# Kernel tuning notes

Hardware: AMD Instinct MI355X
Metric: run time of the kernel (lower is better)

## Reference

```python
import jax, jax.numpy as jnp
import numpy as np

NUM_HEADS = 12
NUM_GROUPS = 4
METRIC_SCALE = 1.0
CLS_MIX = 1.0
MEAN_MIX = 0.5
ROUTER_SCALE = 1.0
DIFF_SCALE = 1.0
B, N, D, HF = 16, 577, 768, 3072


def _ln(x, g, b, eps=1e-5):
    mu = jnp.mean(x, axis=-1, keepdims=True)
    var = jnp.mean(jnp.square(x - mu), axis=-1, keepdims=True)
    return (x - mu) * jax.lax.rsqrt(var + eps) * g + b


def setup_inputs() -> dict:
    key = jax.random.key(0)
    ks = iter(jax.random.split(key, 16))
    w = lambda shape, std: jax.random.normal(next(ks), shape, jnp.float32) * std
    return {
        "x": w((B, N, D), 1.0),
        "ln1_g": jnp.ones((D,)), "ln1_b": jnp.zeros((D,)),
        "ad_ln_g": jnp.ones((D,)), "ad_ln_b": jnp.zeros((D,)),
        "ad_w": w((D, D), 0.02),
        "w_qkv": w((D, 3 * D), 0.02),
        "w_proj": w((D, D), 0.02), "b_proj": jnp.zeros((D,)),
        "ln2_g": jnp.ones((D,)), "ln2_b": jnp.zeros((D,)),
        "fc1_w": w((D, HF), 0.02), "fc1_b": jnp.zeros((HF,)),
        "fc2_w": w((HF, D), 0.02), "fc2_b": jnp.zeros((D,)),
        "r_ln_g": jnp.ones((HF,)), "r_ln_b": jnp.zeros((HF,)),
        "r_proj_w": w((2 * HF, NUM_GROUPS), 0.02), "r_proj_b": jnp.zeros((NUM_GROUPS,)),
        "r_gate_w": w((2 * HF, 1), 0.02), "r_gate_b": jnp.full((1,), -2.0),
        "r_scale": jnp.full((NUM_GROUPS,), 0.1),
        "d_ln_g": jnp.ones((HF,)), "d_ln_b": jnp.zeros((HF,)),
        "d_out_w": w((HF, HF), 0.005),
        "d_gate_w": w((HF, 1), 0.02), "d_gate_b": jnp.full((1,), -1.5),
    }


def reference(x, ln1_g, ln1_b, ad_ln_g, ad_ln_b, ad_w, w_qkv, w_proj, b_proj,
              ln2_g, ln2_b, fc1_w, fc1_b, fc2_w, fc2_b,
              r_ln_g, r_ln_b, r_proj_w, r_proj_b, r_gate_w, r_gate_b, r_scale,
              d_ln_g, d_ln_b, d_out_w, d_gate_w, d_gate_b):
    b, n, d = x.shape
    hd = d // NUM_HEADS
    # ---- GeoAttention (pre-norm) ----
    h = _ln(x, ln1_g, ln1_b)
    # metric adapter: residual LN+Linear (SharedAttentionMetricAdapter)
    metric_h = h + METRIC_SCALE * (_ln(h, ad_ln_g, ad_ln_b) @ ad_w)
    # q,k from metric path; v from plain path (asymmetric Q/K vs V)
    qk = metric_h @ w_qkv[:, : 2 * d]                # [b,n,2d]
    v = h @ w_qkv[:, 2 * d :]                        # [b,n,d]
    q = qk[..., :d].reshape(b, n, NUM_HEADS, hd).transpose(0, 2, 1, 3)
    k = qk[..., d:].reshape(b, n, NUM_HEADS, hd).transpose(0, 2, 1, 3)
    v = v.reshape(b, n, NUM_HEADS, hd).transpose(0, 2, 1, 3)
    attn = jax.nn.softmax(jnp.einsum("bhnd,bhmd->bhnm", q, k) * (hd ** -0.5), axis=-1)
    out = jnp.einsum("bhnm,bhmd->bhnd", attn, v).transpose(0, 2, 1, 3).reshape(b, n, d)
    x = x + out @ w_proj + b_proj
    # ---- GeoMlp (pre-norm) ----
    h2 = _ln(x, ln2_g, ln2_b)
    hid = h2 @ fc1_w + fc1_b                         # [b,n,HF]
    # GroupCompetitionRouter on hidden
    rn = _ln(hid, r_ln_g, r_ln_b)
    summary = jnp.concatenate([CLS_MIX * rn[:, 0], MEAN_MIX * jnp.mean(rn[:, 1:], axis=1)], axis=-1)  # [b,2HF]
    wts = jax.nn.softmax(summary @ r_proj_w + r_proj_b, axis=-1)       # [b,G]
    gate = jax.nn.sigmoid(summary @ r_gate_w + r_gate_b)               # [b,1]
    centered = wts * float(NUM_GROUPS) - 1.0
    grouped = hid.reshape(b, n, NUM_GROUPS, HF // NUM_GROUPS)
    scale = 1.0 + ROUTER_SCALE * gate[:, None, :, None] * r_scale[None, None, :, None] * centered[:, None, :, None]
    hid = (grouped * scale).reshape(b, n, HF)
    # TokenDiffusionMixer on hidden
    dn = _ln(hid, d_ln_g, d_ln_b)
    tr = dn / jnp.maximum(jnp.linalg.norm(dn, axis=-1, keepdims=True), 1e-12)
    aff = jax.nn.softmax(jnp.einsum("bnc,bmc->bnm", tr, tr) * (HF ** -0.5), axis=-1)
    diffusion = jnp.einsum("bnm,bmc->bnc", aff, dn) - dn
    dgate = jax.nn.sigmoid(dn[:, 0] @ d_gate_w + d_gate_b)             # [b,1]
    hid = hid + DIFF_SCALE * dgate[:, :, None] * (diffusion @ d_out_w)
    # activation + fc2
    hid = jax.nn.gelu(hid, approximate=False)
    return x + hid @ fc2_w + fc2_b
```

## Files before the change

kernel.cpp:

```cpp
#include <hip/hip_runtime.h>
#include <math.h>

typedef unsigned short u16;
typedef unsigned int   u32;
typedef __attribute__((ext_vector_type(4))) float f32x4;
typedef __attribute__((ext_vector_type(4))) u32   u32x4;

#define DEV __device__ __forceinline__
#define AS1 __attribute__((address_space(1)))
#define AS3 __attribute__((address_space(3)))

DEV float b2f(u16 u){ u32 x = ((u32)u)<<16; float f; __builtin_memcpy(&f,&x,4); return f; }
DEV u16 f2b(float f){ u32 x; __builtin_memcpy(&x,&f,4); u32 r = x + 0x7FFFu + ((x>>16)&1u); return (u16)(r>>16); }

DEV float ldf(const float* p, long i){ return p[i]; }
DEV float ldf(const u16*   p, long i){ return b2f(p[i]); }

DEV void gload16(const u16* g, u16* l){
  __builtin_amdgcn_global_load_lds((const AS1 u32*)(const void*)g,
                                   (AS3 u32*)(void*)l, 16, 0, 0);
}

DEV float wave_sum(float v){
#pragma unroll
  for(int o=32;o;o>>=1) v += __shfl_down(v,o,64);
  return v;
}
DEV float wave_max(float v){
#pragma unroll
  for(int o=32;o;o>>=1) v = fmaxf(v, __shfl_down(v,o,64));
  return v;
}
DEV float block_sum(float v, float* tmp){
  v = wave_sum(v);
  if((threadIdx.x&63)==0) tmp[threadIdx.x>>6]=v;
  __syncthreads();
  float r = tmp[0]+tmp[1]+tmp[2]+tmp[3];
  __syncthreads();
  return r;
}
DEV float block_max(float v, float* tmp){
  v = wave_max(v);
  if((threadIdx.x&63)==0) tmp[threadIdx.x>>6]=v;
  __syncthreads();
  float r = fmaxf(fmaxf(tmp[0],tmp[1]),fmaxf(tmp[2],tmp[3]));
  __syncthreads();
  return r;
}

template<typename TI>
__global__ void transpose_pad(const TI* __restrict__ in, u16* __restrict__ out,
                              int R, int C, int Rpad, long strideI, long strideO){
  __shared__ u16 t[32][33];
  in  += (long)blockIdx.z*strideI;
  out += (long)blockIdx.z*strideO;
  int tx = threadIdx.x & 31, ty = threadIdx.x >> 5;
  int bc = blockIdx.x*32, br = blockIdx.y*32;
#pragma unroll
  for(int i=0;i<32;i+=8){
    int r = br+ty+i, c = bc+tx;
    float v = (r<R && c<C) ? ldf(in,(long)r*C+c) : 0.f;
    t[ty+i][tx] = f2b(v);
  }
  __syncthreads();
#pragma unroll
  for(int i=0;i<32;i+=8){
    int c = bc+ty+i, r = br+tx;
    if(c<C && r<Rpad) out[(long)c*Rpad + r] = t[tx][ty+i];
  }
}

template<typename TI>
__global__ void ln_rows(const TI* __restrict__ x, const float* __restrict__ g,
                        const float* __restrict__ b, u16* __restrict__ y, int W){
  __shared__ float tmp[4];
  long base=(long)blockIdx.x*W;
  float s=0.f, ss=0.f;
  for(int c=threadIdx.x;c<W;c+=256){ float v=ldf(x,base+c); s+=v; ss+=v*v; }
  s=block_sum(s,tmp); ss=block_sum(ss,tmp);
  float mu=s/W;
  float rstd=rsqrtf(fmaxf(ss/W-mu*mu,0.f)+1e-5f);
  for(int c=threadIdx.x;c<W;c+=256){
    float v=ldf(x,base+c);
    y[base+c]=f2b((v-mu)*rstd*g[c]+b[c]);
  }
}

__global__ void row_stats(const u16* __restrict__ x, float* __restrict__ stats, int W){
  __shared__ float tmp[4];
  long base=(long)blockIdx.x*W;
  float s=0.f,ss=0.f;
  for(int c=threadIdx.x;c<W;c+=256){ float v=b2f(x[base+c]); s+=v; ss+=v*v; }
  s=block_sum(s,tmp); ss=block_sum(ss,tmp);
  if(threadIdx.x==0){
    float mu=s/W;
    stats[2*(long)blockIdx.x]=mu;
    stats[2*(long)blockIdx.x+1]=rsqrtf(fmaxf(ss/W-mu*mu,0.f)+1e-5f);
  }
}

__global__ void dn_kernel(const u16* __restrict__ x, const float* __restrict__ g,
                          const float* __restrict__ b, const float* __restrict__ scalef,
                          u16* __restrict__ dn, float* __restrict__ rn){
  const int W=3072;
  __shared__ float tmp[4];
  __shared__ u16 rowb[3072];
  long row=(long)blockIdx.x;
  long base=row*(long)W;
  int bz=(int)(row/577);
  float s=0.f,ss=0.f;
  for(int c=threadIdx.x;c<W;c+=256){
    float sc=scalef[bz*4 + ((c>>8)/3)];
    float v=b2f(x[base+c])*sc;
    rowb[c]=f2b(v);
    s+=v; ss+=v*v;
  }
  s=block_sum(s,tmp); ss=block_sum(ss,tmp);
  float mu=s/W;
  float rstd=rsqrtf(fmaxf(ss/W-mu*mu,0.f)+1e-5f);
  float sq=0.f;
  for(int c=threadIdx.x;c<W;c+=256){
    float v=(b2f(rowb[c])-mu)*rstd*g[c]+b[c];
    sq+=v*v;
  }
  sq=block_sum(sq,tmp);
  float r=1.f/fmaxf(sqrtf(sq),1e-12f);
  for(int c=threadIdx.x;c<W;c+=256){
    float v=(b2f(rowb[c])-mu)*rstd*g[c]+b[c];
    dn[base+c]=f2b(v);
  }
  if(threadIdx.x==0) rn[blockIdx.x]=r;
}

__global__ void softmax_rows(u16* __restrict__ S, int W, int Wp,
                             const float* __restrict__ rs, int rpb, float alpha){
  __shared__ float tmp[4];
  long row = blockIdx.x;
  u16* p = S + row*(long)Wp;
  float rowscale = alpha;
  const float* rsb = nullptr;
  if(rs){ long bt=row/rpb; int m=(int)(row%rpb); rsb = rs + bt*(long)rpb; rowscale *= rsb[m]; }
  float mx=-3e38f;
  for(int c=threadIdx.x;c<W;c+=256){
    float v=b2f(p[c])*rowscale; if(rs) v*=rsb[c];
    mx=fmaxf(mx,v);
  }
  mx=block_max(mx,tmp);
  float sm=0.f;
  for(int c=threadIdx.x;c<W;c+=256){
    float v=b2f(p[c])*rowscale; if(rs) v*=rsb[c];
    sm+=__expf(v-mx);
  }
  sm=block_sum(sm,tmp);
  float inv=1.f/sm;
  for(int c=threadIdx.x;c<W;c+=256){
    float v=b2f(p[c])*rowscale; if(rs) v*=rsb[c];
    p[c]=f2b(__expf(v-mx)*inv);
  }
  for(int c=W+threadIdx.x;c<Wp;c+=256) p[c]=0;
}

__global__ void split_heads(const u16* __restrict__ qk, u16* __restrict__ qh, u16* __restrict__ kh){
  int i = blockIdx.x*256+threadIdx.x;
  if(i >= 16*577*12*8) return;
  int dv = i&7; int h=(i>>3)%12; int bn=i/96;
  int b=bn/577, n=bn%577;
  long src=(long)bn*1536 + h*64 + dv*8;
  long dst=((long)((b*12+h)*577+n))*64 + dv*8;
  *(u32x4*)(qh+dst) = *(const u32x4*)(qk+src);
  *(u32x4*)(kh+dst) = *(const u32x4*)(qk+src+768);
}
__global__ void merge_heads(const u16* __restrict__ aoh, u16* __restrict__ aout){
  int i = blockIdx.x*256+threadIdx.x;
  if(i >= 16*577*12*8) return;
  int dv=i&7; int h=(i>>3)%12; int bn=i/96;
  int b=bn/577, n=bn%577;
  long dst=(long)bn*768 + h*64 + dv*8;
  long src=((long)((b*12+h)*577+n))*64 + dv*8;
  *(u32x4*)(aout+dst) = *(const u32x4*)(aoh+src);
}
__global__ void make_vT(const u16* __restrict__ v, u16* __restrict__ vT){
  long i = (long)blockIdx.x*256+threadIdx.x;
  if(i >= (long)192*64*608) return;
  int n=(int)(i%608); long q=i/608; int d=(int)(q&63); int bh=(int)(q>>6);
  int b=bh/12, h=bh%12;
  u16 val=0;
  if(n<577) val = v[((long)(b*577+n))*768 + h*64 + d];
  vT[i]=val;
}

__global__ void summary_kernel(const u16* __restrict__ hid, const float* __restrict__ stats,
                               const float* __restrict__ rg, const float* __restrict__ rb,
                               float* __restrict__ summ){
  int b=blockIdx.y;
  int c=blockIdx.x*256+threadIdx.x;
  const u16* hb=hid+(size_t)b*577*3072;
  const float* st=stats+(size_t)b*577*2;
  float g=rg[c], be=rb[c];
  float cls=(b2f(hb[c])-st[0])*st[1]*g+be;
  float acc=0.f;
  for(int n=1;n<577;n++) acc += (b2f(hb[(size_t)n*3072+c])-st[2*n])*st[2*n+1];
  summ[(size_t)b*6144+c]        = 1.0f*cls;
  summ[(size_t)b*6144+3072+c]   = 0.5f*(g*(acc*(1.f/576.f))+be);
}

__global__ void router_kernel(const float* __restrict__ summ, const float* __restrict__ pw,
                              const float* __restrict__ pb, const float* __restrict__ gw,
                              const float* __restrict__ gb, const float* __restrict__ rsc,
                              float* __restrict__ scalef){
  __shared__ float tmp[4];
  int b=blockIdx.x;
  float a0=0,a1=0,a2=0,a3=0,a4=0;
  for(int c=threadIdx.x;c<6144;c+=256){
    float sv=summ[(size_t)b*6144+c];
    a0+=sv*pw[c*4+0]; a1+=sv*pw[c*4+1]; a2+=sv*pw[c*4+2]; a3+=sv*pw[c*4+3];
    a4+=sv*gw[c];
  }
  a0=block_sum(a0,tmp); a1=block_sum(a1,tmp); a2=block_sum(a2,tmp);
  a3=block_sum(a3,tmp); a4=block_sum(a4,tmp);
  if(threadIdx.x==0){
    float l0=a0+pb[0], l1=a1+pb[1], l2=a2+pb[2], l3=a3+pb[3];
    float mx=fmaxf(fmaxf(l0,l1),fmaxf(l2,l3));
    float e0=__expf(l0-mx),e1=__expf(l1-mx),e2=__expf(l2-mx),e3=__expf(l3-mx);
    float s=e0+e1+e2+e3;
    float gate=1.f/(1.f+__expf(-(a4+gb[0])));
    float w0=e0/s,w1=e1/s,w2=e2/s,w3=e3/s;
    scalef[b*4+0]=1.f+gate*rsc[0]*(4.f*w0-1.f);
    scalef[b*4+1]=1.f+gate*rsc[1]*(4.f*w1-1.f);
    scalef[b*4+2]=1.f+gate*rsc[2]*(4.f*w2-1.f);
    scalef[b*4+3]=1.f+gate*rsc[3]*(4.f*w3-1.f);
  }
}

__global__ void dgate_kernel(const u16* __restrict__ dn, const float* __restrict__ gw,
                             const float* __restrict__ gb, float* __restrict__ dgate){
  __shared__ float tmp[4];
  int b=blockIdx.x;
  const u16* row = dn + (size_t)b*577*3072;
  float a=0.f;
  for(int c=threadIdx.x;c<3072;c+=256) a+=b2f(row[c])*gw[c];
  a=block_sum(a,tmp);
  if(threadIdx.x==0) dgate[b]=1.f/(1.f+__expf(-(a+gb[0])));
}

constexpr int F_BIAS=1, F_RES=2, F_GELU=4, F_GATE=8, F_RESF32=16, F_OUTF32=32, F_SCRES=64;

DEV int swz(int u){ int row=u>>2, sl=u&3; return row*4 + (sl ^ ((row>>1)&3)); }

template<int FLAGS>
__global__ __launch_bounds__(256,2) void gemm_bt(
  const u16* __restrict__ A, long lda, long szA,
  const u16* __restrict__ B, long ldb, long szB,
  void* __restrict__ Cv, long ldc, long szC,
  const float* __restrict__ bias,
  const void* __restrict__ resv, long ldr, long szR, float res_scale,
  const float* __restrict__ gate,
  float alpha, int M, int N, int K, int NX, int NY)
{
  __shared__ alignas(16) u16 shA[128*32];
  __shared__ alignas(16) u16 shB[128*32];
  const int nwg = (int)gridDim.x;
  const int orig = (int)blockIdx.x;
  const int q = nwg>>3, r = nwg&7;
  const int xcd = orig&7, idx = orig>>3;
  const int wg = (xcd<r ? xcd*(q+1) : r*(q+1)+(xcd-r)*q) + idx;
  const int bx = wg % NX; const int t_ = wg / NX;
  const int by = t_ % NY; const int z  = t_ / NY;

  A += (long)z*szA; B += (long)z*szB;
  const int tid=threadIdx.x, lane=tid&63, wid=tid>>6;
  const int wr=wid>>1, wc=wid&1;
  const long m0=(long)bx*128, n0=(long)by*128;
  f32x4 acc[4][4];
#pragma unroll
  for(int i=0;i<4;i++)
#pragma unroll
    for(int j=0;j<4;j++){ f32x4 zv={0.f,0.f,0.f,0.f}; acc[i][j]=zv; }

  const int lr = lane>>2, lsl = lane&3;
  const u16* pA[2]; const u16* pB[2]; u16* lA[2]; u16* lB[2];
#pragma unroll
  for(int i=0;i<2;i++){
    int ra = wid*32 + i*16 + lr;
    int kc = (lsl ^ ((ra>>1)&3))*8;
    long gr = m0+ra; if(gr>=M) gr=M-1;
    long gb = n0+ra; if(gb>=N) gb=N-1;
    pA[i] = A + gr*lda + kc;
    pB[i] = B + gb*ldb + kc;
    lA[i] = shA + (wid*32 + i*16)*32;
    lB[i] = shB + (wid*32 + i*16)*32;
  }

  for(int k0=0;k0<K;k0+=32){
    __syncthreads();
#pragma unroll
    for(int i=0;i<2;i++){
      gload16(pA[i]+k0, lA[i]);
      gload16(pB[i]+k0, lB[i]);
    }
    __syncthreads();
    const int ks = lane>>4, rr = lane&15;
    u32x4 av[4], bv[4];
#pragma unroll
    for(int mi=0;mi<4;mi++) av[mi] = ((const u32x4*)shA)[swz((wr*64+mi*16+rr)*4+ks)];
#pragma unroll
    for(int ni=0;ni<4;ni++) bv[ni] = ((const u32x4*)shB)[swz((wc*64+ni*16+rr)*4+ks)];
#pragma unroll
    for(int mi=0;mi<4;mi++)
#pragma unroll
      for(int ni=0;ni<4;ni++)
        asm volatile("v_mfma_f32_16x16x32_bf16 %0, %1, %2, %0"
                     : "+v"(acc[mi][ni]) : "v"(av[mi]), "v"(bv[ni]));
  }
  const float* resf = (const float*)resv + (long)z*szR;
  const u16*   resh = (const u16*)resv   + (long)z*szR;
  float* Cf = (float*)Cv + (long)z*szC;
  u16*   Ch = (u16*)Cv   + (long)z*szC;
  float gv = (FLAGS&F_GATE)? gate[z] : 1.f;
#pragma unroll
  for(int mi=0;mi<4;mi++){
#pragma unroll
    for(int ni=0;ni<4;ni++){
      long c0 = n0 + wc*64 + ni*16 + (lane&15);
      if(c0>=N) continue;
      float bb = (FLAGS&F_BIAS)? bias[c0] : 0.f;
#pragma unroll
      for(int r2=0;r2<4;r2++){
        long rw = m0 + wr*64 + mi*16 + (lane>>4)*4 + r2;
        if(rw>=M) continue;
        float t = acc[mi][ni][r2]*alpha*gv + bb;
        if(FLAGS&F_RES){
          float rvv = (FLAGS&F_RESF32)? resf[rw*ldr+c0] : b2f(resh[rw*ldr+c0]);
          t += res_scale*rvv;
        }
        if(FLAGS&F_GELU) t = 0.5f*t*(1.f+erff(t*0.70710678118654752f));
        if(FLAGS&F_OUTF32) Cf[rw*ldc+c0]=t;
        else               Ch[rw*ldc+c0]=f2b(t);
      }
    }
  }
}

static inline int gpack(int M,int N,int nb,int& NX,int& NY){
  NX=(M+127)/128; NY=(N+127)/128; return NX*NY*nb;
}

template<int FLAGS>
__global__ __launch_bounds__(512,2) void gemm256(
  const u16* __restrict__ A, long lda,
  const u16* __restrict__ B, long ldb,
  u16* __restrict__ C, long ldc,
  const float* __restrict__ bias,
  const u16* __restrict__ res, long ldr,
  const float* __restrict__ gate, const float* __restrict__ scres,
  float irpz, float alpha, int M, int N, int K, int NX)
{
  __shared__ alignas(16) u16 smem[65536];
  char* sm=(char*)smem;
  const int nwg=(int)gridDim.x, orig=(int)blockIdx.x;
  const int qq=nwg>>3, rr8=nwg&7, xcd=orig&7, idx=orig>>3;
  const int wg=(xcd<rr8? xcd*(qq+1): rr8*(qq+1)+(xcd-rr8)*qq)+idx;
  const int bx=wg%NX, by=wg/NX;
  const long m0=(long)bx*256, n0=(long)by*256;
  const int tid=threadIdx.x, lane=tid&63, wid=tid>>6;
  const int wr=wid>>2, wc=wid&3, l15=lane&15, ks=lane>>4;

  f32x4 acc[8][4];
#pragma unroll
  for(int i=0;i<8;i++)
#pragma unroll
    for(int j=0;j<4;j++){ f32x4 zv={0.f,0.f,0.f,0.f}; acc[i][j]=zv; }

  const u16 *sA[2][2], *sB[2][2];
  int dstj[2];
#pragma unroll
  for(int j=0;j<2;j++){
    int u=j*512+tid, row=u>>3;
    long co=(long)(((u&7)^(row&7))*8);
    dstj[j]=u*16;
#pragma unroll
    for(int h=0;h<2;h++){
      long gr=m0+h*128+row; if(gr>=M) gr=M-1;
      long gb=n0+h*128+row; if(gb>=N) gb=N-1;
      sA[h][j]=A+gr*lda+co;
      sB[h][j]=B+gb*ldb+co;
    }
  }
  int xsl[2]; xsl[0]=((ks^(l15&7))<<4); xsl[1]=(((4+ks)^(l15&7))<<4);
  const int arow = wr*16384 + l15*128;
  int brow[4];
#pragma unroll
  for(int nj=0;nj<4;nj++){ int n=wc*64+nj*16; brow[nj]=32768+(n>>7)*16384+((n&127)+l15)*128; }
  const int NT=K>>6;

#define STG(P,mat,h,kt,bf) { \
  gload16(P[h][0]+(long)(kt)*64,(u16*)(sm+(bf)*65536+(mat)*32768+(h)*16384+dstj[0])); \
  gload16(P[h][1]+(long)(kt)*64,(u16*)(sm+(bf)*65536+(mat)*32768+(h)*16384+dstj[1])); }
#define BAR() { asm volatile("":::"memory"); __builtin_amdgcn_s_barrier(); asm volatile("":::"memory"); }
#define MFMA16(A0,KB) { \
  __builtin_amdgcn_s_setprio(1); \
  _Pragma("unroll") for(int i_=0;i_<4;i_++) \
  _Pragma("unroll") for(int j_=0;j_<4;j_++) \
    asm volatile("v_mfma_f32_16x16x32_bf16 %0, %1, %2, %0" \
                 :"+v"(acc[(A0)+i_][j_]):"v"(av[i_]),"v"(bv[KB][j_])); \
  __builtin_amdgcn_s_setprio(0); }

  STG(sB,1,0,0,0); STG(sB,1,1,0,0); STG(sA,0,0,0,0); STG(sA,0,1,0,0);
  if(NT>1){ STG(sB,1,0,1,1); STG(sB,1,1,1,1); STG(sA,0,0,1,1); }
  if(NT>1) asm volatile("s_waitcnt vmcnt(6)":::"memory");
  else     asm volatile("s_waitcnt vmcnt(0)":::"memory");
  BAR();

  u32x4 av[4], bv[2][4];
  for(int t=0;t<NT;++t){
    const int cur=t&1, nxt=cur^1;
    const char* bp = sm + cur*65536;
    if(t+1<NT) STG(sA,0,1,t+1,nxt);
#pragma unroll
    for(int kk=0;kk<2;kk++)
#pragma unroll
      for(int nj=0;nj<4;nj++) bv[kk][nj]=*(const u32x4*)(bp+brow[nj]+xsl[kk]);
#pragma unroll
    for(int i=0;i<4;i++) av[i]=*(const u32x4*)(bp+arow+i*2048+xsl[0]);
    BAR();
    MFMA16(0,0);
    BAR();
    if(t+2<NT) STG(sB,1,0,t+2,cur);
#pragma unroll
    for(int i=0;i<4;i++) av[i]=*(const u32x4*)(bp+arow+(4+i)*2048+xsl[0]);
    BAR();
    MFMA16(4,0);
    BAR();
    if(t+2<NT) STG(sB,1,1,t+2,cur);
#pragma unroll
    for(int i=0;i<4;i++) av[i]=*(const u32x4*)(bp+arow+i*2048+xsl[1]);
    BAR();
    MFMA16(0,1);
    BAR();
    if(t+2<NT) STG(sA,0,0,t+2,cur);
#pragma unroll
    for(int i=0;i<4;i++) av[i]=*(const u32x4*)(bp+arow+(4+i)*2048+xsl[1]);
    if(t+2<NT) asm volatile("s_waitcnt vmcnt(6)":::"memory");
    else       asm volatile("s_waitcnt vmcnt(0)":::"memory");
    BAR();
    MFMA16(4,1);
    BAR();
  }
#undef STG
#undef BAR
#undef MFMA16

#pragma unroll
  for(int mf=0;mf<8;mf++){
#pragma unroll
    for(int j=0;j<4;j++){
      long c0 = n0 + wc*64 + j*16 + l15;
      float bb=(FLAGS&F_BIAS)? bias[c0]:0.f;
      int cg=((int)(c0>>8))/3;
#pragma unroll
      for(int r2=0;r2<4;r2++){
        long rw = m0 + wr*128 + mf*16 + ks*4 + r2;
        if(rw>=M) continue;
        float t=acc[mf][j][r2]*alpha;
        if(FLAGS&(F_GATE|F_SCRES)){
          int z=(int)(((float)rw+0.5f)*irpz);
          if(FLAGS&F_GATE) t*=gate[z];
          if(FLAGS&F_SCRES) t += scres[z*4+cg]*b2f(res[rw*ldr+c0]);
        } else if(FLAGS&F_RES){
          t += b2f(res[rw*ldr+c0]);
        }
        t+=bb;
        if(FLAGS&F_GELU) t=0.5f*t*(1.f+erff(t*0.70710678118654752f));
        C[rw*ldc+c0]=f2b(t);
      }
    }
  }
}

extern "C" void kernel_launch(void* const* d_in, const int* in_sizes, int n_in,
                              void* d_out, int out_size, void* d_ws, size_t ws_size,
                              hipStream_t stream){
  const int BNr=16*577;
  const float* x      = (const float*)d_in[0];
  const float* ln1_g  = (const float*)d_in[1];
  const float* ln1_b  = (const float*)d_in[2];
  const float* ad_ln_g= (const float*)d_in[3];
  const float* ad_ln_b= (const float*)d_in[4];
  const float* ad_w   = (const float*)d_in[5];
  const float* w_qkv  = (const float*)d_in[6];
  const float* w_proj = (const float*)d_in[7];
  const float* b_proj = (const float*)d_in[8];
  const float* ln2_g  = (const float*)d_in[9];
  const float* ln2_b  = (const float*)d_in[10];
  const float* fc1_w  = (const float*)d_in[11];
  const float* fc1_b  = (const float*)d_in[12];
  const float* fc2_w  = (const float*)d_in[13];
  const float* fc2_b  = (const float*)d_in[14];
  const float* r_ln_g = (const float*)d_in[15];
  const float* r_ln_b = (const float*)d_in[16];
  const float* r_proj_w=(const float*)d_in[17];
  const float* r_proj_b=(const float*)d_in[18];
  const float* r_gate_w=(const float*)d_in[19];
  const float* r_gate_b=(const float*)d_in[20];
  const float* r_scale =(const float*)d_in[21];
  const float* d_ln_g = (const float*)d_in[22];
  const float* d_ln_b = (const float*)d_in[23];
  const float* d_outw = (const float*)d_in[24];
  const float* d_gate_w=(const float*)d_in[25];
  const float* d_gate_b=(const float*)d_in[26];

  char* ws=(char*)d_ws;
  size_t off=0;
  auto take=[&](size_t nb){ size_t r=off; off=(off+nb+255)&~(size_t)255; return r; };
  auto al  =[&](size_t v){ return (v+255)&~(size_t)255; };
  const size_t o_qkvT = take((size_t)2304*768*2);
  const size_t o_adT  = take((size_t)768*768*2);
  const size_t o_projT= take((size_t)768*768*2);
  const size_t o_fc1T = take((size_t)3072*768*2);
  const size_t o_fc2T = take((size_t)768*3072*2);
  const size_t o_doutT= take((size_t)3072*3072*2);
  const size_t o_x2   = take((size_t)BNr*768*4);
  const size_t o_hid  = take((size_t)BNr*3072*2);
  const size_t o_stats= take((size_t)BNr*2*4);
  const size_t o_rn   = take((size_t)BNr*4);
  const size_t o_sum  = take((size_t)16*6144*4);
  const size_t o_scalef=take(64*4);
  const size_t o_dg   = take(64);
  const size_t o_h    = take((size_t)BNr*768*2);
  const size_t o_lnh  = take((size_t)BNr*768*2);
  const size_t o_metric=take((size_t)BNr*768*2);
  const size_t o_qk   = take((size_t)BNr*1536*2);
  const size_t o_v    = take((size_t)BNr*768*2);
  const size_t o_qh   = take((size_t)192*577*64*2);
  const size_t o_kh   = take((size_t)192*577*64*2);
  const size_t o_vT   = take((size_t)192*64*608*2);
  (void)o_v; (void)o_vT; (void)ws_size; (void)in_sizes; (void)n_in; (void)out_size;
  const size_t o_S    = o_qk;
  const size_t o_aoh  = o_metric;
  const size_t o_aout = o_h;
  const size_t o_h2   = o_lnh;
  const size_t o_dn   = o_h;
  const size_t o_aff  = al(o_dn + (size_t)BNr*3072*2);
  const size_t o_dnTb = al(o_aff + (size_t)16*577*608*2);
  const size_t o_diff = al(o_dnTb + (size_t)4*3072*608*2);
  const size_t o_hact = o_dn;

  u16* qkvT=(u16*)(ws+o_qkvT); u16* adT=(u16*)(ws+o_adT); u16* projT=(u16*)(ws+o_projT);
  u16* fc1T=(u16*)(ws+o_fc1T); u16* fc2T=(u16*)(ws+o_fc2T); u16* doutT=(u16*)(ws+o_doutT);
  float* x2=(float*)(ws+o_x2); u16* hid=(u16*)(ws+o_hid);
  float* stats=(float*)(ws+o_stats); float* rn=(float*)(ws+o_rn);
  float* summ=(float*)(ws+o_sum); float* scalef=(float*)(ws+o_scalef); float* dgate=(float*)(ws+o_dg);
  u16* hbuf=(u16*)(ws+o_h); u16* lnh=(u16*)(ws+o_lnh); u16* metric=(u16*)(ws+o_metric);
  u16* qkbuf=(u16*)(ws+o_qk); u16* vbuf=(u16*)(ws+o_v);
  u16* qh=(u16*)(ws+o_qh); u16* kh=(u16*)(ws+o_kh); u16* vT=(u16*)(ws+o_vT);
  u16* Sc=(u16*)(ws+o_S); u16* aoh=(u16*)(ws+o_aoh); u16* aout=(u16*)(ws+o_aout);
  u16* h2=(u16*)(ws+o_h2);
  u16* dn=(u16*)(ws+o_dn); u16* aff=(u16*)(ws+o_aff); u16* dnTb=(u16*)(ws+o_dnTb);
  u16* diff=(u16*)(ws+o_diff); u16* hact=(u16*)(ws+o_hact);

  dim3 blk(256), blk5(512);
  int NX, NY, ng;
  transpose_pad<float><<<dim3(72,24,1),blk,0,stream>>>(w_qkv, qkvT, 768,2304,768, 0,0);
  transpose_pad<float><<<dim3(24,24,1),blk,0,stream>>>(ad_w,  adT,  768,768, 768, 0,0);
  transpose_pad<float><<<dim3(24,24,1),blk,0,stream>>>(w_proj,projT,768,768, 768, 0,0);
  transpose_pad<float><<<dim3(96,24,1),blk,0,stream>>>(fc1_w, fc1T, 768,3072,768, 0,0);
  transpose_pad<float><<<dim3(24,96,1),blk,0,stream>>>(fc2_w, fc2T, 3072,768,3072,0,0);
  transpose_pad<float><<<dim3(96,96,1),blk,0,stream>>>(d_outw,doutT,3072,3072,3072,0,0);
  ln_rows<float><<<BNr,blk,0,stream>>>(x, ln1_g, ln1_b, hbuf, 768);
  ln_rows<u16>  <<<BNr,blk,0,stream>>>(hbuf, ad_ln_g, ad_ln_b, lnh, 768);
  ng=gpack(BNr,768,1,NX,NY);
  gemm_bt<F_RES><<<ng,blk,0,stream>>>(lnh,768,0, adT,768,0, metric,768,0,
      nullptr, hbuf,768,0, 1.f, nullptr, 1.f, BNr,768,768, NX,NY);
  gemm256<0><<<dim3(37*6),blk5,0,stream>>>(metric,768, qkvT,768, qkbuf,1536,
      nullptr, nullptr,0, nullptr,nullptr, 0.f, 1.f, BNr,1536,768, 37);
  ng=gpack(BNr,768,1,NX,NY);
  gemm_bt<0><<<ng,blk,0,stream>>>(hbuf,768,0, qkvT+(size_t)1536*768,768,0, vbuf,768,0,
      nullptr, nullptr,0,0,0.f, nullptr, 1.f, BNr,768,768, NX,NY);
  split_heads<<<3462,blk,0,stream>>>(qkbuf, qh, kh);
  make_vT<<<29184,blk,0,stream>>>(vbuf, vT);
  for(int c=0;c<6;c++){
    const u16* qc=qh+(size_t)c*32*577*64;
    const u16* kc=kh+(size_t)c*32*577*64;
    ng=gpack(577,577,32,NX,NY);
    gemm_bt<0><<<ng,blk,0,stream>>>(qc,64,(long)577*64, kc,64,(long)577*64,
        Sc,608,(long)577*608, nullptr, nullptr,0,0,0.f, nullptr, 0.125f, 577,577,64, NX,NY);
    softmax_rows<<<32*577,blk,0,stream>>>(Sc,577,608, nullptr,577, 1.f);
    ng=gpack(577,64,32,NX,NY);
    gemm_bt<0><<<ng,blk,0,stream>>>(Sc,608,(long)577*608, vT+(size_t)c*32*64*608,608,(long)64*608,
        aoh+(size_t)c*32*577*64,64,(long)577*64, nullptr, nullptr,0,0,0.f, nullptr, 1.f, 577,64,608, NX,NY);
  }
  merge_heads<<<3462,blk,0,stream>>>(aoh, aout);
  ng=gpack(BNr,768,1,NX,NY);
  gemm_bt<F_RES|F_BIAS|F_RESF32|F_OUTF32><<<ng,blk,0,stream>>>(aout,768,0, projT,768,0,
      x2,768,0, b_proj, x,768,0, 1.f, nullptr, 1.f, BNr,768,768, NX,NY);
  ln_rows<float><<<BNr,blk,0,stream>>>(x2, ln2_g, ln2_b, h2, 768);
  gemm256<F_BIAS><<<dim3(37*12),blk5,0,stream>>>(h2,768, fc1T,768, hid,3072,
      fc1_b, nullptr,0, nullptr,nullptr, 0.f, 1.f, BNr,3072,768, 37);
  row_stats<<<BNr,blk,0,stream>>>(hid, stats, 3072);
  summary_kernel<<<dim3(12,16),blk,0,stream>>>(hid, stats, r_ln_g, r_ln_b, summ);
  router_kernel<<<16,blk,0,stream>>>(summ, r_proj_w, r_proj_b, r_gate_w, r_gate_b, r_scale, scalef);
  dn_kernel<<<BNr,blk,0,stream>>>(hid, d_ln_g, d_ln_b, scalef, dn, rn);
  dgate_kernel<<<16,blk,0,stream>>>(dn, d_gate_w, d_gate_b, dgate);
  ng=gpack(577,577,16,NX,NY);
  gemm_bt<0><<<ng,blk,0,stream>>>(dn,3072,(long)577*3072, dn,3072,(long)577*3072,
      aff,608,(long)577*608, nullptr, nullptr,0,0,0.f, nullptr, 1.f, 577,577,3072, NX,NY);
  softmax_rows<<<BNr,blk,0,stream>>>(aff,577,608, rn,577, 0.01804219634f);
  for(int g4=0; g4<4; ++g4){
    transpose_pad<u16><<<dim3(96,19,4),blk,0,stream>>>(dn+(size_t)g4*4*577*3072, dnTb,
        577,3072,608, (long)577*3072, (long)3072*608);
    ng=gpack(577,3072,4,NX,NY);
    gemm_bt<F_RES><<<ng,blk,0,stream>>>(aff+(size_t)g4*4*577*608,608,(long)577*608,
        dnTb,608,(long)3072*608, diff+(size_t)g4*4*577*3072,3072,(long)577*3072,
        nullptr, dn+(size_t)g4*4*577*3072,3072,(long)577*3072, -1.f, nullptr, 1.f, 577,3072,608, NX,NY);
  }
  gemm256<F_GELU|F_GATE|F_SCRES><<<dim3(37*12),blk5,0,stream>>>(diff,3072, doutT,3072,
      hact,3072, nullptr, hid,3072, dgate, scalef, 1.f/577.f, 1.f, BNr,3072,3072, 37);
  ng=gpack(BNr,768,1,NX,NY);
  gemm_bt<F_RES|F_BIAS|F_RESF32|F_OUTF32><<<ng,blk,0,stream>>>(hact,3072,0,
      fc2T,3072,0, d_out,768,0, fc2_b, x2,768,0, 1.f, nullptr, 1.f, BNr,768,3072, NX,NY);
}
```

Baseline: 1.509 ms.

## Reorder GEMM tile mapping to N-fastest and restructure gemm256 prefetch schedule

Both GEMM kernels now map consecutive workgroups along the N (column-tile) dimension first, so blocks that share an A row-panel run close together and can reuse it from cache. The gemm256 prefetch schedule is reworked: both A halves of the next tile are issued at the start of each iteration and the B halves two tiles ahead, with the waitcnt tightened to match. gemm256 also gains optional f32 residual/output paths, which are not used by any current launch. The new issue order changes how load latency overlaps the MFMA work, and it now loads tile 1 unconditionally, which assumes K spans at least two k-tiles.

```diff
diff --git a/kernel.cpp b/kernel.cpp
--- a/kernel.cpp
+++ b/kernel.cpp
@@ -264,8 +264,8 @@
   const int q = nwg>>3, r = nwg&7;
   const int xcd = orig&7, idx = orig>>3;
   const int wg = (xcd<r ? xcd*(q+1) : r*(q+1)+(xcd-r)*q) + idx;
-  const int bx = wg % NX; const int t_ = wg / NX;
-  const int by = t_ % NY; const int z  = t_ / NY;
+  const int by = wg % NY; const int t_ = wg / NY;
+  const int bx = t_ % NX; const int z  = t_ / NX;
 
   A += (long)z*szA; B += (long)z*szB;
   const int tid=threadIdx.x, lane=tid&63, wid=tid>>6;
@@ -349,18 +349,18 @@
 __global__ __launch_bounds__(512,2) void gemm256(
   const u16* __restrict__ A, long lda,
   const u16* __restrict__ B, long ldb,
-  u16* __restrict__ C, long ldc,
+  void* __restrict__ Cv, long ldc,
   const float* __restrict__ bias,
-  const u16* __restrict__ res, long ldr,
+  const void* __restrict__ resv, long ldr,
   const float* __restrict__ gate, const float* __restrict__ scres,
-  float irpz, float alpha, int M, int N, int K, int NX)
+  float irpz, float alpha, int M, int N, int K, int NY)
 {
   __shared__ alignas(16) u16 smem[65536];
   char* sm=(char*)smem;
   const int nwg=(int)gridDim.x, orig=(int)blockIdx.x;
   const int qq=nwg>>3, rr8=nwg&7, xcd=orig&7, idx=orig>>3;
   const int wg=(xcd<rr8? xcd*(qq+1): rr8*(qq+1)+(xcd-rr8)*qq)+idx;
-  const int bx=wg%NX, by=wg/NX;
+  const int by=wg%NY, bx=wg/NY;
   const long m0=(long)bx*256, n0=(long)by*256;
   const int tid=threadIdx.x, lane=tid&63, wid=tid>>6;
   const int wr=wid>>2, wc=wid&3, l15=lane&15, ks=lane>>4;
@@ -405,17 +405,16 @@
                  :"+v"(acc[(A0)+i_][j_]):"v"(av[i_]),"v"(bv[KB][j_])); \
   __builtin_amdgcn_s_setprio(0); }
 
-  STG(sB,1,0,0,0); STG(sB,1,1,0,0); STG(sA,0,0,0,0); STG(sA,0,1,0,0);
-  if(NT>1){ STG(sB,1,0,1,1); STG(sB,1,1,1,1); STG(sA,0,0,1,1); }
-  if(NT>1) asm volatile("s_waitcnt vmcnt(6)":::"memory");
-  else     asm volatile("s_waitcnt vmcnt(0)":::"memory");
+  STG(sA,0,0,0,0); STG(sA,0,1,0,0); STG(sB,1,0,0,0); STG(sB,1,1,0,0);
+  STG(sB,1,0,1,1); STG(sB,1,1,1,1);
+  asm volatile("s_waitcnt vmcnt(4)":::"memory");
   BAR();
 
   u32x4 av[4], bv[2][4];
   for(int t=0;t<NT;++t){
     const int cur=t&1, nxt=cur^1;
     const char* bp = sm + cur*65536;
-    if(t+1<NT) STG(sA,0,1,t+1,nxt);
+    if(t+1<NT){ STG(sA,0,0,t+1,nxt); STG(sA,0,1,t+1,nxt); }
 #pragma unroll
     for(int kk=0;kk<2;kk++)
 #pragma unroll
@@ -425,22 +424,21 @@
     BAR();
     MFMA16(0,0);
     BAR();
+#pragma unroll
+    for(int i=0;i<4;i++) av[i]=*(const u32x4*)(bp+arow+(4+i)*2048+xsl[0]);
+    BAR();
+    MFMA16(4,0);
+    BAR();
     if(t+2<NT) STG(sB,1,0,t+2,cur);
 #pragma unroll
-    for(int i=0;i<4;i++) av[i]=*(const u32x4*)(bp+arow+(4+i)*2048+xsl[0]);
-    BAR();
-    MFMA16(4,0);
+    for(int i=0;i<4;i++) av[i]=*(const u32x4*)(bp+arow+i*2048+xsl[1]);
+    BAR();
+    MFMA16(0,1);
     BAR();
     if(t+2<NT) STG(sB,1,1,t+2,cur);
 #pragma unroll
-    for(int i=0;i<4;i++) av[i]=*(const u32x4*)(bp+arow+i*2048+xsl[1]);
-    BAR();
-    MFMA16(0,1);
-    BAR();
-    if(t+2<NT) STG(sA,0,0,t+2,cur);
-#pragma unroll
     for(int i=0;i<4;i++) av[i]=*(const u32x4*)(bp+arow+(4+i)*2048+xsl[1]);
-    if(t+2<NT) asm volatile("s_waitcnt vmcnt(6)":::"memory");
+    if(t+2<NT) asm volatile("s_waitcnt vmcnt(4)":::"memory");
     else       asm volatile("s_waitcnt vmcnt(0)":::"memory");
     BAR();
     MFMA16(4,1);
@@ -450,6 +448,8 @@
 #undef BAR
 #undef MFMA16
 
+  const float* resf=(const float*)resv; const u16* resh=(const u16*)resv;
+  float* Cf=(float*)Cv; u16* Ch=(u16*)Cv;
 #pragma unroll
   for(int mf=0;mf<8;mf++){
 #pragma unroll
@@ -465,13 +465,15 @@
         if(FLAGS&(F_GATE|F_SCRES)){
           int z=(int)(((float)rw+0.5f)*irpz);
           if(FLAGS&F_GATE) t*=gate[z];
-          if(FLAGS&F_SCRES) t += scres[z*4+cg]*b2f(res[rw*ldr+c0]);
+          if(FLAGS&F_SCRES) t += scres[z*4+cg]*b2f(resh[rw*ldr+c0]);
         } else if(FLAGS&F_RES){
-          t += b2f(res[rw*ldr+c0]);
+          float rvv=(FLAGS&F_RESF32)? resf[rw*ldr+c0] : b2f(resh[rw*ldr+c0]);
+          t += rvv;
         }
         t+=bb;
         if(FLAGS&F_GELU) t=0.5f*t*(1.f+erff(t*0.70710678118654752f));
-        C[rw*ldc+c0]=f2b(t);
+        if(FLAGS&F_OUTF32) Cf[rw*ldc+c0]=t;
+        else               Ch[rw*ldc+c0]=f2b(t);
       }
     }
   }
@@ -572,7 +574,7 @@
   gemm_bt<F_RES><<<ng,blk,0,stream>>>(lnh,768,0, adT,768,0, metric,768,0,
       nullptr, hbuf,768,0, 1.f, nullptr, 1.f, BNr,768,768, NX,NY);
   gemm256<0><<<dim3(37*6),blk5,0,stream>>>(metric,768, qkvT,768, qkbuf,1536,
-      nullptr, nullptr,0, nullptr,nullptr, 0.f, 1.f, BNr,1536,768, 37);
+      nullptr, nullptr,0, nullptr,nullptr, 0.f, 1.f, BNr,1536,768, 6);
   ng=gpack(BNr,768,1,NX,NY);
   gemm_bt<0><<<ng,blk,0,stream>>>(hbuf,768,0, qkvT+(size_t)1536*768,768,0, vbuf,768,0,
       nullptr, nullptr,0,0,0.f, nullptr, 1.f, BNr,768,768, NX,NY);
@@ -595,7 +597,7 @@
       x2,768,0, b_proj, x,768,0, 1.f, nullptr, 1.f, BNr,768,768, NX,NY);
   ln_rows<float><<<BNr,blk,0,stream>>>(x2, ln2_g, ln2_b, h2, 768);
   gemm256<F_BIAS><<<dim3(37*12),blk5,0,stream>>>(h2,768, fc1T,768, hid,3072,
-      fc1_b, nullptr,0, nullptr,nullptr, 0.f, 1.f, BNr,3072,768, 37);
+      fc1_b, nullptr,0, nullptr,nullptr, 0.f, 1.f, BNr,3072,768, 12);
   row_stats<<<BNr,blk,0,stream>>>(hid, stats, 3072);
   summary_kernel<<<dim3(12,16),blk,0,stream>>>(hid, stats, r_ln_g, r_ln_b, summ);
   router_kernel<<<16,blk,0,stream>>>(summ, r_proj_w, r_proj_b, r_gate_w, r_gate_b, r_scale, scalef);
@@ -614,7 +616,7 @@
         nullptr, dn+(size_t)g4*4*577*3072,3072,(long)577*3072, -1.f, nullptr, 1.f, 577,3072,608, NX,NY);
   }
   gemm256<F_GELU|F_GATE|F_SCRES><<<dim3(37*12),blk5,0,stream>>>(diff,3072, doutT,3072,
-      hact,3072, nullptr, hid,3072, dgate, scalef, 1.f/577.f, 1.f, BNr,3072,3072, 37);
+      hact,3072, nullptr, hid,3072, dgate, scalef, 1.f/577.f, 1.f, BNr,3072,3072, 12);
   ng=gpack(BNr,768,1,NX,NY);
   gemm_bt<F_RES|F_BIAS|F_RESF32|F_OUTF32><<<ng,blk,0,stream>>>(hact,3072,0,
       fc2T,3072,0, d_out,768,0, fc2_b, x2,768,0, 1.f, nullptr, 1.f, BNr,768,3072, NX,NY);
```

Measured after the change: 1.501 ms. About the same (-0.5%).
